# Performance work log

Hardware: AMD Instinct MI355X
Metric: run time of the kernel (lower is better)

## Reference

```python
import jax, jax.numpy as jnp
import numpy as np

N, D_IN, D_OUT = 8192, 1024, 1024

def setup_inputs() -> dict:
    key = jax.random.key(0)
    kx, kq, kk, kv = jax.random.split(key, 4)
    # Linear weights stored as [in_dim, out_dim] (torch stores [out,in]; we pre-transpose)
    s = 1.0 / np.sqrt(D_IN)
    return {
        "x": jax.random.normal(kx, (N, D_IN), dtype=jnp.float32),
        "Wq": jax.random.uniform(kq, (D_IN, D_OUT), dtype=jnp.float32, minval=-s, maxval=s),
        "Wk": jax.random.uniform(kk, (D_IN, D_OUT), dtype=jnp.float32, minval=-s, maxval=s),
        "Wv": jax.random.uniform(kv, (D_IN, D_OUT), dtype=jnp.float32, minval=-s, maxval=s),
    }

def reference(x, Wq, Wk, Wv):
    # Faithful to source: query_w = keys_L(x), key_w = queries_L(x) -- a name swap
    # that is just a relabeling of independent random weights. The earlier
    # parameter matmuls in the source are dead code (overwritten) and omitted.
    q = x @ Wk          # [N, D_OUT]
    k = x @ Wq          # [N, D_OUT]
    v = x @ Wv          # [N, D_OUT]
    scores = (q @ k.T) / jnp.sqrt(jnp.asarray(D_OUT, dtype=q.dtype))  # [N, N]
    weights = jax.nn.softmax(scores, axis=-1)
    return weights @ v  # [N, D_OUT]
```

## Files before the change

### kernel.cpp

```cpp
#include <hip/hip_runtime.h>
#include <hip/hip_bf16.h>
#include <stdint.h>

typedef __bf16 v8bf __attribute__((ext_vector_type(8)));
typedef __bf16 v4bf __attribute__((ext_vector_type(4)));
typedef float  v4f  __attribute__((ext_vector_type(4)));

#define AS1 __attribute__((address_space(1)))
#define AS3 __attribute__((address_space(3)))

__device__ __forceinline__ void load16_lds(const void* g, void* l) {
  __builtin_amdgcn_global_load_lds((const AS1 uint32_t*)g, (AS3 uint32_t*)l, 16, 0, 0);
}

__global__ __launch_bounds__(256) void k_cvt_x(const float* __restrict__ x,
                                               __bf16* __restrict__ xb,
                                               float* __restrict__ rowsum) {
  size_t i = ((size_t)blockIdx.x * 256 + threadIdx.x) * 4;
  float4 f = *(const float4*)(x + i);
  v4bf b; b[0] = (__bf16)f.x; b[1] = (__bf16)f.y; b[2] = (__bf16)f.z; b[3] = (__bf16)f.w;
  *(v4bf*)(xb + i) = b;
  if (blockIdx.x == 0) {
    #pragma unroll
    for (int z = 0; z < 8; z++)
      *(float4*)(rowsum + ((size_t)threadIdx.x * 8 + z) * 4) =
          make_float4(0.f, 0.f, 0.f, 0.f);
  }
}

__global__ __launch_bounds__(256) void k_wtrans(const float* __restrict__ W,
                                                __bf16* __restrict__ Wt) {
  __shared__ float tile[64][65];
  int r0 = blockIdx.x * 64, c0 = blockIdx.y * 64;
  int t = threadIdx.x;
  #pragma unroll
  for (int p = 0; p < 16; p++) {
    int idx = p * 256 + t; int rr = idx >> 6, cc = idx & 63;
    tile[rr][cc] = W[(size_t)(r0 + rr) * 1024 + c0 + cc];
  }
  __syncthreads();
  #pragma unroll
  for (int p = 0; p < 16; p++) {
    int idx = p * 256 + t; int rr = idx >> 6, cc = idx & 63;
    Wt[(size_t)(c0 + rr) * 1024 + r0 + cc] = (__bf16)tile[cc][rr];
  }
}

__global__ __launch_bounds__(256) void k_vtrans(const __bf16* __restrict__ V,
                                                __bf16* __restrict__ Vt) {
  __shared__ __bf16 tile[64][66];
  int r0 = blockIdx.x * 64, c0 = blockIdx.y * 64;
  int t = threadIdx.x;
  #pragma unroll
  for (int p = 0; p < 16; p++) {
    int idx = p * 256 + t; int rr = idx >> 6, cc = idx & 63;
    tile[rr][cc] = V[(size_t)(r0 + rr) * 1024 + c0 + cc];
  }
  __syncthreads();
  #pragma unroll
  for (int p = 0; p < 16; p++) {
    int idx = p * 256 + t; int rr = idx >> 6, cc = idx & 63;
    Vt[(size_t)(c0 + rr) * 8192 + r0 + cc] = tile[cc][rr];
  }
}

template <int EPI>
__global__ __launch_bounds__(256, 2) void gemm_nt(
    const __bf16* __restrict__ A, const __bf16* __restrict__ B,
    void* __restrict__ Cout, int M, int N, int K,
    __bf16* __restrict__ qp, __bf16* __restrict__ kp, __bf16* __restrict__ vp,
    float* __restrict__ rowsum, const float* __restrict__ rsum_in)
{
  __shared__ __bf16 Asm[128 * 64];
  __shared__ __bf16 Bsm[128 * 64];
  const int tid = threadIdx.x;
  const int wave = tid >> 6, lane = tid & 63;
  const size_t m0 = (size_t)blockIdx.x * 128;
  const size_t n0 = (size_t)blockIdx.y * 128;
  const int wm = (wave >> 1) * 64, wn = (wave & 1) * 64;

  v4f acc[4][4];
  #pragma unroll
  for (int i = 0; i < 4; i++)
    #pragma unroll
    for (int j = 0; j < 4; j++) acc[i][j] = (v4f)0.f;

  const int srow8   = lane >> 3;
  const int sgchunk = (lane & 7) ^ srow8;
  const int fr  = lane & 15;
  const int hi  = lane >> 4;
  const int flo = lane & 7;
  const size_t sK = (size_t)K;

  for (int k0 = 0; k0 < K; k0 += 64) {
    #pragma unroll
    for (int p = 0; p < 4; p++) {
      const int seg = p * 4 + wave;
      const int row = seg * 8 + srow8;
      load16_lds(A + (m0 + row) * sK + (size_t)k0 + sgchunk * 8, Asm + seg * 512);
      load16_lds(B + (n0 + row) * sK + (size_t)k0 + sgchunk * 8, Bsm + seg * 512);
    }
    __syncthreads();
    #pragma unroll
    for (int h = 0; h < 2; h++) {
      const int slot = ((h << 2) | hi) ^ flo;
      v8bf a_frag[4], b_frag[4];
      #pragma unroll
      for (int i = 0; i < 4; i++)
        a_frag[i] = *(const v8bf*)(Asm + (wm + i * 16 + fr) * 64 + slot * 8);
      #pragma unroll
      for (int j = 0; j < 4; j++)
        b_frag[j] = *(const v8bf*)(Bsm + (wn + j * 16 + fr) * 64 + slot * 8);
      #pragma unroll
      for (int i = 0; i < 4; i++)
        #pragma unroll
        for (int j = 0; j < 4; j++)
          acc[i][j] = __builtin_amdgcn_mfma_f32_16x16x32_bf16(a_frag[i], b_frag[j], acc[i][j], 0, 0, 0);
    }
    __syncthreads();
  }

  const int er = (lane >> 4) * 4;
  const int ec = lane & 15;

  if (EPI == 3) {
    float rpart[4][4];
    #pragma unroll
    for (int i = 0; i < 4; i++)
      #pragma unroll
      for (int r = 0; r < 4; r++) rpart[i][r] = 0.f;
    #pragma unroll
    for (int i = 0; i < 4; i++)
      #pragma unroll
      for (int j = 0; j < 4; j++) {
        const size_t col = n0 + wn + j * 16 + ec;
        #pragma unroll
        for (int r = 0; r < 4; r++) {
          const size_t rowg = m0 + wm + i * 16 + er + r;
          float e = __expf(acc[i][j][r]);
          ((__bf16*)Cout)[rowg * (size_t)N + col] = (__bf16)e;
          rpart[i][r] += e;
        }
      }
    #pragma unroll
    for (int i = 0; i < 4; i++)
      #pragma unroll
      for (int r = 0; r < 4; r++) {
        float s = rpart[i][r];
        s += __shfl_xor(s, 1); s += __shfl_xor(s, 2);
        s += __shfl_xor(s, 4); s += __shfl_xor(s, 8);
        if (ec == 0) atomicAdd(&rowsum[m0 + wm + i * 16 + er + r], s);
      }
    return;
  }

  if (EPI == 0) {
    #pragma unroll
    for (int i = 0; i < 4; i++)
      #pragma unroll
      for (int r = 0; r < 4; r++) {
        const size_t rowg = m0 + wm + i * 16 + er + r;
        const float rv = 1.0f / rsum_in[rowg];
        #pragma unroll
        for (int j = 0; j < 4; j++) {
          const size_t col = n0 + wn + j * 16 + ec;
          ((float*)Cout)[rowg * (size_t)N + col] = acc[i][j][r] * rv;
        }
      }
    return;
  }

  #pragma unroll
  for (int i = 0; i < 4; i++)
    #pragma unroll
    for (int j = 0; j < 4; j++) {
      const size_t col = n0 + wn + j * 16 + ec;
      #pragma unroll
      for (int r = 0; r < 4; r++) {
        const size_t rowg = m0 + wm + i * 16 + er + r;
        float val = acc[i][j][r];
        const int buf = (int)(col >> 10);
        const size_t cc = col & 1023;
        __bf16* dst = (buf == 0) ? qp : ((buf == 1) ? kp : vp);
        if (buf == 0) val *= 0.03125f;
        dst[rowg * 1024 + cc] = (__bf16)val;
      }
    }
}

extern "C" void kernel_launch(void* const* d_in, const int* in_sizes, int n_in,
                              void* d_out, int out_size, void* d_ws, size_t ws_size,
                              hipStream_t stream) {
  const float* x  = (const float*)d_in[0];
  const float* Wq = (const float*)d_in[1];
  const float* Wk = (const float*)d_in[2];
  const float* Wv = (const float*)d_in[3];
  float* out = (float*)d_out;

  const size_t N = 8192, D = 1024;
  char* ws = (char*)d_ws;
  size_t off = 0;
  __bf16* xb = (__bf16*)(ws + off); off += N * D * 2;
  __bf16* wt = (__bf16*)(ws + off); off += 3 * D * D * 2;
  __bf16* q  = (__bf16*)(ws + off); off += N * D * 2;
  __bf16* k  = (__bf16*)(ws + off); off += N * D * 2;
  __bf16* v  = (__bf16*)(ws + off); off += N * D * 2;
  __bf16* vt = (__bf16*)(ws + off); off += N * D * 2;
  __bf16* S  = (__bf16*)(ws + off); off += N * N * 2;
  float* rowsum = (float*)(ws + off); off += N * 4;
  if (ws_size < off) return;

  k_cvt_x<<<dim3(8192), dim3(256), 0, stream>>>(x, xb, rowsum);
  k_wtrans<<<dim3(16, 16), dim3(256), 0, stream>>>(Wk, wt);
  k_wtrans<<<dim3(16, 16), dim3(256), 0, stream>>>(Wq, wt + D * D);
  k_wtrans<<<dim3(16, 16), dim3(256), 0, stream>>>(Wv, wt + 2 * D * D);
  gemm_nt<2><<<dim3(64, 24), dim3(256), 0, stream>>>(xb, wt, nullptr, 8192, 3072, 1024, q, k, v, nullptr, nullptr);
  k_vtrans<<<dim3(128, 16), dim3(256), 0, stream>>>(v, vt);
  gemm_nt<3><<<dim3(64, 64), dim3(256), 0, stream>>>(q, k, S, 8192, 8192, 1024, nullptr, nullptr, nullptr, rowsum, nullptr);
  gemm_nt<0><<<dim3(64, 8), dim3(256), 0, stream>>>(S, vt, out, 8192, 1024, 8192, nullptr, nullptr, nullptr, nullptr, rowsum);
}
```

Before: 448.5 us.

## Replace QK^T exp GEMM with 256x256 double-buffered pipelined MFMA kernel

The Q·K^T score GEMM with fused exp and rowsum moves from the generic 128x128 single-buffered kernel to a dedicated 256x256 tile kernel with 512 threads. Its LDS buffers are double-buffered, and global-to-LDS loads for upcoming k-steps are interleaved with four MFMA quadrants per step, separated by barriers and s_setprio. The aim is to hide load latency and raise arithmetic intensity on the largest GEMM. In exchange it uses 128KB of LDS and more registers per block, which may limit occupancy. The launch_bounds of 2 blocks per CU may not be reachable.

```diff
diff --git a/kernel.cpp b/kernel.cpp
--- a/kernel.cpp
+++ b/kernel.cpp
@@ -123,37 +123,6 @@
   const int er = (lane >> 4) * 4;
   const int ec = lane & 15;
 
-  if (EPI == 3) {
-    float rpart[4][4];
-    #pragma unroll
-    for (int i = 0; i < 4; i++)
-      #pragma unroll
-      for (int r = 0; r < 4; r++) rpart[i][r] = 0.f;
-    #pragma unroll
-    for (int i = 0; i < 4; i++)
-      #pragma unroll
-      for (int j = 0; j < 4; j++) {
-        const size_t col = n0 + wn + j * 16 + ec;
-        #pragma unroll
-        for (int r = 0; r < 4; r++) {
-          const size_t rowg = m0 + wm + i * 16 + er + r;
-          float e = __expf(acc[i][j][r]);
-          ((__bf16*)Cout)[rowg * (size_t)N + col] = (__bf16)e;
-          rpart[i][r] += e;
-        }
-      }
-    #pragma unroll
-    for (int i = 0; i < 4; i++)
-      #pragma unroll
-      for (int r = 0; r < 4; r++) {
-        float s = rpart[i][r];
-        s += __shfl_xor(s, 1); s += __shfl_xor(s, 2);
-        s += __shfl_xor(s, 4); s += __shfl_xor(s, 8);
-        if (ec == 0) atomicAdd(&rowsum[m0 + wm + i * 16 + er + r], s);
-      }
-    return;
-  }
-
   if (EPI == 0) {
     #pragma unroll
     for (int i = 0; i < 4; i++)
@@ -185,6 +154,190 @@
         if (buf == 0) val *= 0.03125f;
         dst[rowg * 1024 + cc] = (__bf16)val;
       }
+    }
+}
+
+__global__ __launch_bounds__(512, 2) void gemm256_exp(
+    const __bf16* __restrict__ A, const __bf16* __restrict__ B,
+    __bf16* __restrict__ Sout, int Ncols, int K,
+    float* __restrict__ rowsum)
+{
+  __shared__ __bf16 Asm[2][256 * 64];
+  __shared__ __bf16 Bsm[2][256 * 64];
+
+  const int tid  = threadIdx.x;
+  const int wave = tid >> 6, lane = tid & 63;
+  const int wm = (wave >> 2) * 128;
+  const int wn = (wave & 3) * 64;
+  const size_t m0 = (size_t)blockIdx.x * 256;
+  const size_t n0 = (size_t)blockIdx.y * 256;
+  const int NT = K >> 6;
+
+  const int srow8   = lane >> 3;
+  const int sgchunk = (lane & 7) ^ srow8;
+  const int fr  = lane & 15;
+  const int hi  = lane >> 4;
+  const int flo = lane & 7;
+  const size_t sK = (size_t)K;
+
+  v4f acc[8][4];
+  #pragma unroll
+  for (int i = 0; i < 8; i++)
+    #pragma unroll
+    for (int j = 0; j < 4; j++) acc[i][j] = (v4f)0.f;
+
+  auto stageA = [&](int v, int R0) {
+    const int kk = (v < NT ? v : NT - 1) * 64;
+    const __bf16* s = A + (m0 + R0 + wave * 8 + srow8) * sK + kk + sgchunk * 8;
+    __bf16* d = &Asm[v & 1][(R0 + wave * 8) * 64];
+    load16_lds(s, d);
+    load16_lds(s + 64 * sK, d + 64 * 64);
+  };
+  auto stageB = [&](int v, int R0) {
+    const int kk = (v < NT ? v : NT - 1) * 64;
+    const __bf16* s = B + (n0 + R0 + wave * 8 + srow8) * sK + kk + sgchunk * 8;
+    __bf16* d = &Bsm[v & 1][(R0 + wave * 8) * 64];
+    load16_lds(s, d);
+    load16_lds(s + 64 * sK, d + 64 * 64);
+  };
+  auto LD = [&](const __bf16* buf, int R, int h) {
+    return *(const v8bf*)(buf + (R + fr) * 64 + ((((h << 2) | hi) ^ flo) * 8));
+  };
+
+  v8bf aLO[4][2], aHI[4][2], bA[2][2], bB[2][2];
+
+  stageA(0, 0); stageA(0, 128);
+  stageB(0, 0); stageB(0, 128);
+  stageB(1, 0); stageB(1, 128);
+  asm volatile("s_waitcnt vmcnt(4)" ::: "memory");
+  __builtin_amdgcn_s_barrier();
+  __builtin_amdgcn_sched_barrier(0);
+  #pragma unroll
+  for (int i = 0; i < 4; i++)
+    #pragma unroll
+    for (int h = 0; h < 2; h++) aLO[i][h] = LD(Asm[0], wm + i * 16, h);
+  #pragma unroll
+  for (int j = 0; j < 2; j++)
+    #pragma unroll
+    for (int h = 0; h < 2; h++) bA[j][h] = LD(Bsm[0], wn + j * 16, h);
+
+  for (int t = 0; t < NT; ++t) {
+    const int c = t & 1;
+    const __bf16* Ab  = Asm[c];
+    const __bf16* Bb  = Bsm[c];
+    const __bf16* Abn = Asm[c ^ 1];
+    const __bf16* Bbn = Bsm[c ^ 1];
+
+    #pragma unroll
+    for (int j = 0; j < 2; j++)
+      #pragma unroll
+      for (int h = 0; h < 2; h++) bB[j][h] = LD(Bb, wn + (j + 2) * 16, h);
+    stageA(t + 1, 0);
+    __builtin_amdgcn_sched_barrier(0);
+    __builtin_amdgcn_s_barrier();
+    __builtin_amdgcn_sched_barrier(0);
+    __builtin_amdgcn_s_setprio(1);
+    #pragma unroll
+    for (int h = 0; h < 2; h++)
+      #pragma unroll
+      for (int i = 0; i < 4; i++)
+        #pragma unroll
+        for (int j = 0; j < 2; j++)
+          acc[i][j] = __builtin_amdgcn_mfma_f32_16x16x32_bf16(aLO[i][h], bA[j][h], acc[i][j], 0, 0, 0);
+    __builtin_amdgcn_s_setprio(0);
+    __builtin_amdgcn_s_barrier();
+
+    #pragma unroll
+    for (int i = 0; i < 4; i++)
+      #pragma unroll
+      for (int h = 0; h < 2; h++) aHI[i][h] = LD(Ab, wm + (i + 4) * 16, h);
+    stageA(t + 1, 128);
+    __builtin_amdgcn_sched_barrier(0);
+    __builtin_amdgcn_s_barrier();
+    __builtin_amdgcn_sched_barrier(0);
+    __builtin_amdgcn_s_setprio(1);
+    #pragma unroll
+    for (int h = 0; h < 2; h++)
+      #pragma unroll
+      for (int i = 0; i < 4; i++)
+        #pragma unroll
+        for (int j = 0; j < 2; j++)
+          acc[i][j + 2] = __builtin_amdgcn_mfma_f32_16x16x32_bf16(aLO[i][h], bB[j][h], acc[i][j + 2], 0, 0, 0);
+    __builtin_amdgcn_s_setprio(0);
+    __builtin_amdgcn_s_barrier();
+
+    stageB(t + 2, 0);
+    __builtin_amdgcn_sched_barrier(0);
+    __builtin_amdgcn_s_barrier();
+    __builtin_amdgcn_sched_barrier(0);
+    __builtin_amdgcn_s_setprio(1);
+    #pragma unroll
+    for (int h = 0; h < 2; h++)
+      #pragma unroll
+      for (int i = 0; i < 4; i++)
+        #pragma unroll
+        for (int j = 0; j < 2; j++)
+          acc[i + 4][j + 2] = __builtin_amdgcn_mfma_f32_16x16x32_bf16(aHI[i][h], bB[j][h], acc[i + 4][j + 2], 0, 0, 0);
+    __builtin_amdgcn_s_setprio(0);
+    asm volatile("s_waitcnt vmcnt(2)" ::: "memory");
+    __builtin_amdgcn_s_barrier();
+    __builtin_amdgcn_sched_barrier(0);
+
+    stageB(t + 2, 128);
+    __builtin_amdgcn_sched_barrier(0);
+    __builtin_amdgcn_s_barrier();
+    __builtin_amdgcn_sched_barrier(0);
+    __builtin_amdgcn_s_setprio(1);
+    #pragma unroll
+    for (int h = 0; h < 2; h++)
+      #pragma unroll
+      for (int i = 0; i < 4; i++)
+        #pragma unroll
+        for (int j = 0; j < 2; j++)
+          acc[i + 4][j] = __builtin_amdgcn_mfma_f32_16x16x32_bf16(aHI[i][h], bA[j][h], acc[i + 4][j], 0, 0, 0);
+    __builtin_amdgcn_s_setprio(0);
+    if (t + 1 < NT) {
+      #pragma unroll
+      for (int i = 0; i < 4; i++)
+        #pragma unroll
+        for (int h = 0; h < 2; h++) aLO[i][h] = LD(Abn, wm + i * 16, h);
+      #pragma unroll
+      for (int j = 0; j < 2; j++)
+        #pragma unroll
+        for (int h = 0; h < 2; h++) bA[j][h] = LD(Bbn, wn + j * 16, h);
+    }
+    __builtin_amdgcn_sched_barrier(0);
+    __builtin_amdgcn_s_barrier();
+  }
+
+  const int er = (lane >> 4) * 4;
+  const int ec = lane & 15;
+  float rpart[8][4];
+  #pragma unroll
+  for (int i = 0; i < 8; i++)
+    #pragma unroll
+    for (int r = 0; r < 4; r++) rpart[i][r] = 0.f;
+  #pragma unroll
+  for (int i = 0; i < 8; i++)
+    #pragma unroll
+    for (int j = 0; j < 4; j++) {
+      const size_t col = n0 + wn + j * 16 + ec;
+      #pragma unroll
+      for (int r = 0; r < 4; r++) {
+        const size_t rowg = m0 + wm + i * 16 + er + r;
+        float e = __expf(acc[i][j][r]);
+        Sout[rowg * (size_t)Ncols + col] = (__bf16)e;
+        rpart[i][r] += e;
+      }
+    }
+  #pragma unroll
+  for (int i = 0; i < 8; i++)
+    #pragma unroll
+    for (int r = 0; r < 4; r++) {
+      float s = rpart[i][r];
+      s += __shfl_xor(s, 1); s += __shfl_xor(s, 2);
+      s += __shfl_xor(s, 4); s += __shfl_xor(s, 8);
+      if (ec == 0) atomicAdd(&rowsum[m0 + wm + i * 16 + er + r], s);
     }
 }
 
@@ -216,6 +369,6 @@
   k_wtrans<<<dim3(16, 16), dim3(256), 0, stream>>>(Wv, wt + 2 * D * D);
   gemm_nt<2><<<dim3(64, 24), dim3(256), 0, stream>>>(xb, wt, nullptr, 8192, 3072, 1024, q, k, v, nullptr, nullptr);
   k_vtrans<<<dim3(128, 16), dim3(256), 0, stream>>>(v, vt);
-  gemm_nt<3><<<dim3(64, 64), dim3(256), 0, stream>>>(q, k, S, 8192, 8192, 1024, nullptr, nullptr, nullptr, rowsum, nullptr);
+  gemm256_exp<<<dim3(32, 32), dim3(512), 0, stream>>>(q, k, S, 8192, 1024, rowsum);
   gemm_nt<0><<<dim3(64, 8), dim3(256), 0, stream>>>(S, vt, out, 8192, 1024, 8192, nullptr, nullptr, nullptr, nullptr, rowsum);
 }
```

New measurement: 450.5 us. About the same (+0.5%).
